# Kernel tuning notes

Measured on AMD Instinct MI355X. Metric: run time of the kernel, lower is better.

## Reference

```python
import jax, jax.numpy as jnp
import numpy as np

HEAD_SIZE = 64

def setup_inputs() -> dict:
    key = jax.random.key(0)
    k1, k2, k3, k4 = jax.random.split(key, 4)
    B, S, D = 8, 2048, 1024
    scale = 1.0 / np.sqrt(D)
    x = jax.random.normal(k1, (B, S, D), dtype=jnp.float32)
    Wk = jax.random.normal(k2, (D, HEAD_SIZE), dtype=jnp.float32) * scale
    Wq = jax.random.normal(k3, (D, HEAD_SIZE), dtype=jnp.float32) * scale
    Wv = jax.random.normal(k4, (D, HEAD_SIZE), dtype=jnp.float32) * scale
    return {"x": x, "Wk": Wk, "Wq": Wq, "Wv": Wv}

def reference(x, Wk, Wq, Wv):
    # x: [B, S, D]; projections to [B, S, H]
    k = jnp.einsum('bsd,dh->bsh', x, Wk)
    q = jnp.einsum('bsd,dh->bsh', x, Wq)
    v = jnp.einsum('bsd,dh->bsh', x, Wv)
    H = q.shape[-1]
    scores = jnp.einsum('bqh,bkh->bqk', q, k) / jnp.sqrt(jnp.float32(H))  # [B,S,S]
    S = scores.shape[-1]
    causal = jnp.tril(jnp.ones((S, S), dtype=bool))
    scores = jnp.where(causal, scores, -jnp.inf)
    attn = jax.nn.softmax(scores, axis=-1)
    z = jnp.einsum('bqk,bkh->bqh', attn, v)  # [B,S,H]
    return z
```

## Files before the change

kernel.cpp:

```cpp
#include <hip/hip_runtime.h>
#include <hip/hip_bf16.h>

#define B_ 8
#define S_ 2048
#define D_ 1024
#define H_ 64

typedef __attribute__((ext_vector_type(8))) short bf16x8;
typedef __attribute__((ext_vector_type(4))) float f32x4;
typedef __attribute__((ext_vector_type(4))) unsigned short u16x4;
typedef unsigned short u16;
typedef unsigned int u32;

#define QSCALE 0.18033688011112042f

static __device__ __forceinline__ u16 f2bf(float f) {
  union { float f; unsigned u; } v; v.f = f;
  unsigned r = v.u + 0x7FFFu + ((v.u >> 16) & 1u);
  return (u16)(r >> 16);
}

__global__ __launch_bounds__(256) void wprep_kernel(const float* __restrict__ Wk,
                                                    const float* __restrict__ Wq,
                                                    const float* __restrict__ Wv,
                                                    u16* __restrict__ Wt) {
  __shared__ float lds[64][65];
  const int wsel = blockIdx.x >> 4;
  const int d0 = (blockIdx.x & 15) << 6;
  const float* W = (wsel == 0) ? Wq : ((wsel == 1) ? Wk : Wv);
  const int cbase = wsel << 6;
  const int tid = threadIdx.x;

#pragma unroll
  for (int e = 0; e < 16; ++e) {
    const int idx = e * 256 + tid;
    const int dd = idx >> 6, h = idx & 63;
    lds[dd][h] = W[(size_t)(d0 + dd) * H_ + h];
  }
  __syncthreads();
#pragma unroll
  for (int e = 0; e < 16; ++e) {
    const int idx = e * 256 + tid;
    const int c = idx >> 6, dd = idx & 63;
    Wt[(size_t)(cbase + c) * D_ + d0 + dd] = f2bf(lds[dd][c]);
  }
}

__global__ __launch_bounds__(512, 4) void qkv_kernel(const float* __restrict__ x,
                                                     const u16* __restrict__ Wt,
                                                     u16* __restrict__ Qb,
                                                     u16* __restrict__ Kb,
                                                     u16* __restrict__ Vt) {
  __shared__ char sh[65536];
  char* const xsb = sh;
  char* const wsb = sh + 16384;

  const int tid = threadIdx.x;
  const int w = tid >> 6;
  const int lane = tid & 63;
  const int r = lane & 15;
  const int g = lane >> 4;
  const int rg = w >> 2;
  const int cg = w & 3;

  const int bpin = blockIdx.x & 7;
  const int jj = blockIdx.x >> 3;
  const long row0 = ((long)bpin * 64 + jj) * 32;

#define STAGE_X(kc, buf)                                                       \
  {                                                                            \
    const char* gb = (const char*)x + (size_t)row0 * 4096 + (size_t)(kc) * 256;\
    const int L = tid * 16;                                                    \
    const int row = L >> 8;                                                    \
    const int sw = (L & 255) ^ ((row & 7) << 4);                               \
    __builtin_amdgcn_global_load_lds(                                          \
        (const __attribute__((address_space(1))) u32*)(gb + (size_t)row * 4096 + sw), \
        (__attribute__((address_space(3))) u32*)(xsb + (buf) * 8192 + L),      \
        16, 0, 0);                                                             \
  }

#define STAGE_W(kc, buf)                                                       \
  {                                                                            \
    const char* gb = (const char*)Wt + (size_t)(kc) * 128;                     \
    _Pragma("unroll") for (int j2 = 0; j2 < 3; ++j2) {                         \
      const int L = j2 * 8192 + tid * 16;                                      \
      const int col = L >> 7;                                                  \
      const int sw = (L & 127) ^ ((col & 7) << 4);                             \
      __builtin_amdgcn_global_load_lds(                                        \
          (const __attribute__((address_space(1))) u32*)(gb + (size_t)col * 2048 + sw), \
          (__attribute__((address_space(3))) u32*)(wsb + (buf) * 24576 + L),   \
          16, 0, 0);                                                           \
    }                                                                          \
  }

  f32x4 acc[3];
#pragma unroll
  for (int nf = 0; nf < 3; ++nf) acc[nf] = (f32x4){0.f, 0.f, 0.f, 0.f};

  STAGE_X(0, 0);
  STAGE_W(0, 0);
  int cur = 0;

  const int rr = rg * 16 + r;
  const int xswz = (rr & 7) << 4;

  for (int kc = 0; kc < 16; ++kc) {
    __syncthreads();
    if (kc < 15) {
      STAGE_X(kc + 1, cur ^ 1);
      STAGE_W(kc + 1, cur ^ 1);
    }
    __builtin_amdgcn_sched_barrier(0);

    const char* xb = xsb + cur * 8192;
    const char* wb = wsb + cur * 24576;
#pragma unroll
    for (int ks = 0; ks < 2; ++ks) {
      const int cb = ks * 128 + g * 32;
      const float4 lo = *(const float4*)(xb + rr * 256 + (cb ^ xswz));
      const float4 hi = *(const float4*)(xb + rr * 256 + ((cb + 16) ^ xswz));
      bf16x8 a;
      a[0] = (short)f2bf(lo.x); a[1] = (short)f2bf(lo.y);
      a[2] = (short)f2bf(lo.z); a[3] = (short)f2bf(lo.w);
      a[4] = (short)f2bf(hi.x); a[5] = (short)f2bf(hi.y);
      a[6] = (short)f2bf(hi.z); a[7] = (short)f2bf(hi.w);
#pragma unroll
      for (int nf = 0; nf < 3; ++nf) {
        const int col = cg * 48 + nf * 16 + r;
        const int wcb = (ks * 64 + g * 16) ^ ((col & 7) << 4);
        const bf16x8 b = *(const bf16x8*)(wb + col * 128 + wcb);
        acc[nf] = __builtin_amdgcn_mfma_f32_16x16x32_bf16(a, b, acc[nf], 0, 0, 0);
      }
    }
    cur ^= 1;
  }
#undef STAGE_W
#undef STAGE_X

  const int bb = bpin;
  const int srow = (int)(row0 & 2047) + rg * 16;
#pragma unroll
  for (int nf = 0; nf < 3; ++nf) {
    const int col = cg * 48 + nf * 16 + r;
    if (col < 64) {
#pragma unroll
      for (int ii = 0; ii < 4; ++ii)
        Qb[(row0 + rg * 16 + 4 * g + ii) * H_ + col] = f2bf(acc[nf][ii] * QSCALE);
    } else if (col < 128) {
#pragma unroll
      for (int ii = 0; ii < 4; ++ii)
        Kb[(row0 + rg * 16 + 4 * g + ii) * H_ + (col - 64)] = f2bf(acc[nf][ii]);
    } else {
      u16x4 vp;
#pragma unroll
      for (int ii = 0; ii < 4; ++ii) vp[ii] = f2bf(acc[nf][ii]);
      *(u16x4*)(Vt + ((size_t)(bb * H_ + (col - 128))) * S_ + srow + 4 * g) = vp;
    }
  }
}

__global__ __launch_bounds__(256, 2) void attn7_kernel(const u16* __restrict__ Qb,
                                                       const u16* __restrict__ Kb,
                                                       const u16* __restrict__ Vt,
                                                       float* __restrict__ out) {
  __shared__ u16 plds[4][16 * 72];
  __shared__ float plo[4][16][68];
  __shared__ float pml[4][2][16];

  const int b = blockIdx.x & 7;
  const int j = blockIdx.x >> 3;
  const int w = threadIdx.x >> 6;
  const int lane = threadIdx.x & 63;
  const int r = lane & 15;
  const int g = lane >> 4;

  const int qt = (w < 2) ? j : (127 - j);
  const int s = w & 1;
  const int q0 = qt << 4;
  const int T = (qt >> 2) + 1;
  const int half = (T + 1) >> 1;
  const int start = s ? half : 0;
  const int end = s ? T : half;

  const u16* Qp = Qb + ((long)(b * S_ + q0 + r)) * H_ + 8 * g;
  const bf16x8 bq0 = *(const bf16x8*)Qp;
  const bf16x8 bq1 = *(const bf16x8*)(Qp + 32);

  const u16* Kbase = Kb + (long)b * S_ * H_ + (long)r * H_ + 8 * g;
  const u16* Vbase = Vt + (long)b * H_ * S_ + (long)r * S_ + 8 * g;

  f32x4 o[4];
#pragma unroll
  for (int nf = 0; nf < 4; ++nf) o[nf] = (f32x4){0.f, 0.f, 0.f, 0.f};
  float m = -INFINITY, l = 0.f;

  u16* pw = plds[w];

  bf16x8 ka[8];
  if (start < end) {
    const int k0 = start << 6;
#pragma unroll
    for (int kf = 0; kf < 4; ++kf) {
      const u16* Kp = Kbase + (long)(k0 + kf * 16) * H_;
      ka[2 * kf] = *(const bf16x8*)(Kp);
      ka[2 * kf + 1] = *(const bf16x8*)(Kp + 32);
    }
  }

  for (int kt = start; kt < end; ++kt) {
    const int k0 = kt << 6;

    f32x4 t4[4];
    __builtin_amdgcn_s_setprio(1);
#pragma unroll
    for (int kf = 0; kf < 4; ++kf) {
      f32x4 t = (f32x4){0.f, 0.f, 0.f, 0.f};
      t = __builtin_amdgcn_mfma_f32_16x16x32_bf16(ka[2 * kf], bq0, t, 0, 0, 0);
      t = __builtin_amdgcn_mfma_f32_16x16x32_bf16(ka[2 * kf + 1], bq1, t, 0, 0, 0);
      t4[kf] = t;
    }
    __builtin_amdgcn_s_setprio(0);

    bf16x8 vv[8];
#pragma unroll
    for (int nf = 0; nf < 4; ++nf) {
      const u16* Vp = Vbase + (long)(nf * 16) * S_ + k0;
      vv[2 * nf] = *(const bf16x8*)(Vp);
      vv[2 * nf + 1] = *(const bf16x8*)(Vp + 32);
    }
    if (kt + 1 < end) {
      const int kn = (kt + 1) << 6;
#pragma unroll
      for (int kf = 0; kf < 4; ++kf) {
        const u16* Kp = Kbase + (long)(kn + kf * 16) * H_;
        ka[2 * kf] = *(const bf16x8*)(Kp);
        ka[2 * kf + 1] = *(const bf16x8*)(Kp + 32);
      }
    }

    if (kt == T - 1) {
#pragma unroll
      for (int kf = 0; kf < 4; ++kf)
#pragma unroll
        for (int i = 0; i < 4; ++i) {
          const int k = k0 + kf * 16 + 4 * g + i;
          if (k > q0 + r) t4[kf][i] = -INFINITY;
        }
    }

    float pm = t4[0][0];
#pragma unroll
    for (int kf = 0; kf < 4; ++kf)
#pragma unroll
      for (int i = 0; i < 4; ++i) pm = fmaxf(pm, t4[kf][i]);
    pm = fmaxf(pm, __shfl_xor(pm, 16));
    pm = fmaxf(pm, __shfl_xor(pm, 32));

    if (__any(pm > m + 8.f)) {
      const float mn = fmaxf(m, pm);
      const float sc = exp2f(m - mn);
      m = mn;
      l *= sc;
      float scr[4];
#pragma unroll
      for (int i = 0; i < 4; ++i) scr[i] = __shfl(sc, 4 * g + i);
#pragma unroll
      for (int nf = 0; nf < 4; ++nf)
#pragma unroll
        for (int i = 0; i < 4; ++i) o[nf][i] *= scr[i];
    }

    float ps = 0.f;
#pragma unroll
    for (int kf = 0; kf < 4; ++kf)
#pragma unroll
      for (int i = 0; i < 4; ++i) {
        const float p = exp2f(t4[kf][i] - m);
        t4[kf][i] = p;
        ps += p;
      }
    ps += __shfl_xor(ps, 16);
    ps += __shfl_xor(ps, 32);
    l += ps;

#pragma unroll
    for (int kf = 0; kf < 4; ++kf) {
      u16x4 pk;
#pragma unroll
      for (int i = 0; i < 4; ++i) pk[i] = f2bf(t4[kf][i]);
      *(u16x4*)(pw + r * 72 + kf * 16 + 4 * g) = pk;
    }

    const bf16x8 pa0 = *(const bf16x8*)(pw + r * 72 + 8 * g);
    const bf16x8 pa1 = *(const bf16x8*)(pw + r * 72 + 32 + 8 * g);

    __builtin_amdgcn_s_setprio(1);
#pragma unroll
    for (int nf = 0; nf < 4; ++nf) {
      o[nf] = __builtin_amdgcn_mfma_f32_16x16x32_bf16(pa0, vv[2 * nf], o[nf], 0, 0, 0);
      o[nf] = __builtin_amdgcn_mfma_f32_16x16x32_bf16(pa1, vv[2 * nf + 1], o[nf], 0, 0, 0);
    }
    __builtin_amdgcn_s_setprio(0);
  }

#pragma unroll
  for (int nf = 0; nf < 4; ++nf)
#pragma unroll
    for (int i = 0; i < 4; ++i)
      plo[w][4 * g + i][nf * 16 + r] = o[nf][i];
  if (g == 0) {
    pml[w][0][r] = m;
    pml[w][1][r] = l;
  }
  __syncthreads();

  const int base = (w >> 1) << 1;
  const int hlf = w & 1;
  const int qq0 = ((base == 0) ? j : (127 - j)) << 4;
#pragma unroll
  for (int rr = 0; rr < 8; ++rr) {
    const int row = hlf * 8 + rr;
    const float mA = pml[base][0][row], mB = pml[base + 1][0][row];
    const float lA = pml[base][1][row], lB = pml[base + 1][1][row];
    const float M = fmaxf(mA, mB);
    const float ea = exp2f(mA - M), eb = exp2f(mB - M);
    const float inv = 1.f / (lA * ea + lB * eb);
    const float oo = plo[base][row][lane] * ea + plo[base + 1][row][lane] * eb;
    out[((long)(b * S_ + qq0 + row)) * H_ + lane] = oo * inv;
  }
}

extern "C" void kernel_launch(void* const* d_in, const int* in_sizes, int n_in,
                              void* d_out, int out_size, void* d_ws, size_t ws_size,
                              hipStream_t stream) {
  const float* x  = (const float*)d_in[0];
  const float* Wk = (const float*)d_in[1];
  const float* Wq = (const float*)d_in[2];
  const float* Wv = (const float*)d_in[3];
  float* out = (float*)d_out;

  u16* Qb = (u16*)d_ws;
  u16* Kb = Qb + (long)B_ * S_ * H_;
  u16* Vt = Kb + (long)B_ * S_ * H_;
  u16* Wt = Vt + (long)B_ * S_ * H_;

  wprep_kernel<<<48, 256, 0, stream>>>(Wk, Wq, Wv, Wt);
  qkv_kernel<<<512, 512, 0, stream>>>(x, Wt, Qb, Kb, Vt);
  attn7_kernel<<<B_ * 64, 256, 0, stream>>>(Qb, Kb, Vt, out);
}
```

Measured before the change: 60.44 us.

## Hold W fragments in registers and split-K the QKV projection across waves

The QKV projection kernel now uses 1024-thread blocks. Each block loads its slice of the transposed bf16 weights into registers once, then streams 16-row chunks of x through double-buffered LDS. The 1024-wide D dimension is split across four wave groups, and their partial sums are reduced through LDS before one group writes Q, K and V. This removes the repeated staging of W through LDS, but adds two barriers per chunk, an LDS reduction, higher register pressure (24 bf16x8 fragments per thread), 128 KB of LDS per block, and half as many blocks.

```diff
diff --git a/kernel.cpp b/kernel.cpp
--- a/kernel.cpp
+++ b/kernel.cpp
@@ -46,117 +46,127 @@
   }
 }
 
-__global__ __launch_bounds__(512, 4) void qkv_kernel(const float* __restrict__ x,
-                                                     const u16* __restrict__ Wt,
-                                                     u16* __restrict__ Qb,
-                                                     u16* __restrict__ Kb,
-                                                     u16* __restrict__ Vt) {
-  __shared__ char sh[65536];
-  char* const xsb = sh;
-  char* const wsb = sh + 16384;
+__global__ __launch_bounds__(1024, 4) void qkv_kernel(const float* __restrict__ x,
+                                                      const u16* __restrict__ Wt,
+                                                      u16* __restrict__ Qb,
+                                                      u16* __restrict__ Kb,
+                                                      u16* __restrict__ Vt) {
+  __shared__ __attribute__((aligned(16))) char xs[2][65536];
 
   const int tid = threadIdx.x;
   const int w = tid >> 6;
   const int lane = tid & 63;
   const int r = lane & 15;
   const int g = lane >> 4;
-  const int rg = w >> 2;
   const int cg = w & 3;
+  const int ks = w >> 2;
 
   const int bpin = blockIdx.x & 7;
   const int jj = blockIdx.x >> 3;
-  const long row0 = ((long)bpin * 64 + jj) * 32;
-
-#define STAGE_X(kc, buf)                                                       \
+
+#define STAGE_X(c, buf)                                                        \
   {                                                                            \
-    const char* gb = (const char*)x + (size_t)row0 * 4096 + (size_t)(kc) * 256;\
-    const int L = tid * 16;                                                    \
-    const int row = L >> 8;                                                    \
-    const int sw = (L & 255) ^ ((row & 7) << 4);                               \
-    __builtin_amdgcn_global_load_lds(                                          \
-        (const __attribute__((address_space(1))) u32*)(gb + (size_t)row * 4096 + sw), \
-        (__attribute__((address_space(3))) u32*)(xsb + (buf) * 8192 + L),      \
-        16, 0, 0);                                                             \
-  }
-
-#define STAGE_W(kc, buf)                                                       \
-  {                                                                            \
-    const char* gb = (const char*)Wt + (size_t)(kc) * 128;                     \
-    _Pragma("unroll") for (int j2 = 0; j2 < 3; ++j2) {                         \
-      const int L = j2 * 8192 + tid * 16;                                      \
-      const int col = L >> 7;                                                  \
-      const int sw = (L & 127) ^ ((col & 7) << 4);                             \
+    const size_t crow = (size_t)bpin * 2048 + (size_t)(jj * 4 + (c)) * 16;     \
+    const char* gb = (const char*)x + crow * 4096;                             \
+    _Pragma("unroll") for (int j = 0; j < 4; ++j) {                            \
+      const int L = j * 16384 + tid * 16;                                      \
+      const int row = L >> 12;                                                 \
+      const int off = (L & 4095) ^ ((row & 7) << 4);                           \
       __builtin_amdgcn_global_load_lds(                                        \
-          (const __attribute__((address_space(1))) u32*)(gb + (size_t)col * 2048 + sw), \
-          (__attribute__((address_space(3))) u32*)(wsb + (buf) * 24576 + L),   \
+          (const __attribute__((address_space(1))) u32*)(gb + (size_t)row * 4096 + off), \
+          (__attribute__((address_space(3))) u32*)(&xs[buf][0] + L),           \
           16, 0, 0);                                                           \
     }                                                                          \
   }
 
-  f32x4 acc[3];
-#pragma unroll
-  for (int nf = 0; nf < 3; ++nf) acc[nf] = (f32x4){0.f, 0.f, 0.f, 0.f};
-
   STAGE_X(0, 0);
-  STAGE_W(0, 0);
+
+  const u16* wbase = Wt + (size_t)(cg * 48 + r) * D_ + ks * 256 + g * 8;
+  bf16x8 wf[3][8];
+#pragma unroll
+  for (int nf = 0; nf < 3; ++nf)
+#pragma unroll
+    for (int s = 0; s < 8; ++s)
+      wf[nf][s] = *(const bf16x8*)(wbase + (size_t)nf * 16 * D_ + s * 32);
+
   int cur = 0;
-
-  const int rr = rg * 16 + r;
-  const int xswz = (rr & 7) << 4;
-
-  for (int kc = 0; kc < 16; ++kc) {
+  const int rsw = (r & 7) << 4;
+
+  for (int c = 0; c < 4; ++c) {
+    const size_t row0 = (size_t)bpin * 2048 + (size_t)(jj * 4 + c) * 16;
+
     __syncthreads();
-    if (kc < 15) {
-      STAGE_X(kc + 1, cur ^ 1);
-      STAGE_W(kc + 1, cur ^ 1);
-    }
-    __builtin_amdgcn_sched_barrier(0);
-
-    const char* xb = xsb + cur * 8192;
-    const char* wb = wsb + cur * 24576;
-#pragma unroll
-    for (int ks = 0; ks < 2; ++ks) {
-      const int cb = ks * 128 + g * 32;
-      const float4 lo = *(const float4*)(xb + rr * 256 + (cb ^ xswz));
-      const float4 hi = *(const float4*)(xb + rr * 256 + ((cb + 16) ^ xswz));
+    if (c < 3) STAGE_X(c + 1, cur ^ 1);
+    __builtin_amdgcn_sched_barrier(0);
+
+    const char* xb = &xs[cur][0];
+    f32x4 a0 = (f32x4){0.f, 0.f, 0.f, 0.f};
+    f32x4 a1 = a0, a2 = a0;
+#pragma unroll
+    for (int s = 0; s < 8; ++s) {
+      const int inrow = ks * 1024 + s * 128 + g * 32;
+      const float4 lo = *(const float4*)(xb + r * 4096 + (inrow ^ rsw));
+      const float4 hi = *(const float4*)(xb + r * 4096 + ((inrow + 16) ^ rsw));
       bf16x8 a;
       a[0] = (short)f2bf(lo.x); a[1] = (short)f2bf(lo.y);
       a[2] = (short)f2bf(lo.z); a[3] = (short)f2bf(lo.w);
       a[4] = (short)f2bf(hi.x); a[5] = (short)f2bf(hi.y);
       a[6] = (short)f2bf(hi.z); a[7] = (short)f2bf(hi.w);
+      a0 = __builtin_amdgcn_mfma_f32_16x16x32_bf16(a, wf[0][s], a0, 0, 0, 0);
+      a1 = __builtin_amdgcn_mfma_f32_16x16x32_bf16(a, wf[1][s], a1, 0, 0, 0);
+      a2 = __builtin_amdgcn_mfma_f32_16x16x32_bf16(a, wf[2][s], a2, 0, 0, 0);
+    }
+
+    asm volatile("s_waitcnt lgkmcnt(0)" ::: "memory");
+    __builtin_amdgcn_sched_barrier(0);
+    __builtin_amdgcn_s_barrier();
+    __builtin_amdgcn_sched_barrier(0);
+
+    float* red = (float*)(&xs[cur][0]);
+    if (ks != 0) {
+      float* dst = red + (((ks - 1) * 4 + cg) * 64 + lane) * 12;
+      *(f32x4*)&dst[0] = a0;
+      *(f32x4*)&dst[4] = a1;
+      *(f32x4*)&dst[8] = a2;
+    }
+    asm volatile("s_waitcnt lgkmcnt(0)" ::: "memory");
+    __builtin_amdgcn_sched_barrier(0);
+    __builtin_amdgcn_s_barrier();
+    __builtin_amdgcn_sched_barrier(0);
+
+    if (ks == 0) {
+#pragma unroll
+      for (int sl = 0; sl < 3; ++sl) {
+        const float* src = red + ((sl * 4 + cg) * 64 + lane) * 12;
+        a0 += *(const f32x4*)&src[0];
+        a1 += *(const f32x4*)&src[4];
+        a2 += *(const f32x4*)&src[8];
+      }
+      const int bb = bpin;
+      const int srow = (int)(row0 & 2047);
+      f32x4 sv[3] = {a0, a1, a2};
 #pragma unroll
       for (int nf = 0; nf < 3; ++nf) {
         const int col = cg * 48 + nf * 16 + r;
-        const int wcb = (ks * 64 + g * 16) ^ ((col & 7) << 4);
-        const bf16x8 b = *(const bf16x8*)(wb + col * 128 + wcb);
-        acc[nf] = __builtin_amdgcn_mfma_f32_16x16x32_bf16(a, b, acc[nf], 0, 0, 0);
+        if (col < 64) {
+#pragma unroll
+          for (int ii = 0; ii < 4; ++ii)
+            Qb[(row0 + 4 * g + ii) * H_ + col] = f2bf(sv[nf][ii] * QSCALE);
+        } else if (col < 128) {
+#pragma unroll
+          for (int ii = 0; ii < 4; ++ii)
+            Kb[(row0 + 4 * g + ii) * H_ + (col - 64)] = f2bf(sv[nf][ii]);
+        } else {
+          u16x4 vp;
+#pragma unroll
+          for (int ii = 0; ii < 4; ++ii) vp[ii] = f2bf(sv[nf][ii]);
+          *(u16x4*)(Vt + ((size_t)(bb * H_ + (col - 128))) * S_ + srow + 4 * g) = vp;
+        }
       }
     }
     cur ^= 1;
   }
-#undef STAGE_W
 #undef STAGE_X
-
-  const int bb = bpin;
-  const int srow = (int)(row0 & 2047) + rg * 16;
-#pragma unroll
-  for (int nf = 0; nf < 3; ++nf) {
-    const int col = cg * 48 + nf * 16 + r;
-    if (col < 64) {
-#pragma unroll
-      for (int ii = 0; ii < 4; ++ii)
-        Qb[(row0 + rg * 16 + 4 * g + ii) * H_ + col] = f2bf(acc[nf][ii] * QSCALE);
-    } else if (col < 128) {
-#pragma unroll
-      for (int ii = 0; ii < 4; ++ii)
-        Kb[(row0 + rg * 16 + 4 * g + ii) * H_ + (col - 64)] = f2bf(acc[nf][ii]);
-    } else {
-      u16x4 vp;
-#pragma unroll
-      for (int ii = 0; ii < 4; ++ii) vp[ii] = f2bf(acc[nf][ii]);
-      *(u16x4*)(Vt + ((size_t)(bb * H_ + (col - 128))) * S_ + srow + 4 * g) = vp;
-    }
-  }
 }
 
 __global__ __launch_bounds__(256, 2) void attn7_kernel(const u16* __restrict__ Qb,
@@ -345,6 +355,6 @@
   u16* Wt = Vt + (long)B_ * S_ * H_;
 
   wprep_kernel<<<48, 256, 0, stream>>>(Wk, Wq, Wv, Wt);
-  qkv_kernel<<<512, 512, 0, stream>>>(x, Wt, Qb, Kb, Vt);
+  qkv_kernel<<<256, 1024, 0, stream>>>(x, Wt, Qb, Kb, Vt);
   attn7_kernel<<<B_ * 64, 256, 0, stream>>>(Qb, Kb, Vt, out);
 }
```

After: 99.47 us. 64.6% more time.
